# Performance work log

Hardware: AMD Instinct MI355X
Metric: run time of the kernel (lower is better)

The kernel has to match this reference:

```python
import jax, jax.numpy as jnp
import numpy as np

T, B, E, H = 1024, 8, 1024, 16
HD = E // H                       # 64
SCALE = float(HD * 1) ** -0.5     # scaling_factor = 1


def setup_inputs() -> dict:
    key = jax.random.key(0)
    ks = jax.random.split(key, 7)
    s = 0.02
    return {
        "query": jax.random.normal(ks[0], (T, B, E), jnp.float32),
        "key_padding_mask": jax.random.bernoulli(ks[1], 0.1, (B, T)),
        "attn_bias": jax.random.normal(ks[2], (1, H, T, T), jnp.float32) * 0.1,
        "wq": jax.random.normal(ks[3], (1, E, E), jnp.float32) * s,
        "wk": jax.random.normal(ks[4], (1, E, E), jnp.float32) * s,
        "wv": jax.random.normal(ks[5], (1, E, E), jnp.float32) * s,
        "wo": jax.random.normal(ks[6], (1, E, E), jnp.float32) * s,
    }


def _group_linear(x, w):
    # x: (T, B, nb*din), w: (nb, din, dout) -> (T, B, nb*dout). nb=1 here.
    t, b, _ = x.shape
    nb, din, dout = w.shape
    y = jnp.einsum('xnd,nde->xne', x.reshape(t * b, nb, din), w)
    return y.reshape(t, b, nb * dout)


def reference(query, key_padding_mask, attn_bias, wq, wk, wv, wo):
    q = _group_linear(query, wq) * SCALE
    k = _group_linear(query, wk)
    v = _group_linear(query, wv)

    # (T, B, E) -> (B*H, T, HD), matching torch view+transpose
    def split_heads(x):
        return x.reshape(T, B * H, HD).transpose(1, 0, 2)

    q, k, v = split_heads(q), split_heads(k), split_heads(v)

    scores = jnp.einsum('bth,bsh->bts', q, k).reshape(B, H, T, T)
    scores = scores + attn_bias
    scores = jnp.where(key_padding_mask[:, None, None, :], -jnp.inf, scores)
    probs = jax.nn.softmax(scores.astype(jnp.float32), axis=-1).astype(query.dtype)

    vh = v.reshape(B, H, T, HD)  # (B*H,T,HD) -> (B,H,S,HD)
    attn = jnp.einsum('bhts,bhsd->tbhd', probs, vh).reshape(T, B, H * HD)
    return _group_linear(attn, wo)
```

## Files before the change

kernel.cpp:

```cpp
#include <hip/hip_runtime.h>


typedef __bf16 bf16x8 __attribute__((ext_vector_type(8)));
typedef float f32x4 __attribute__((ext_vector_type(4)));

#define LOG2E 1.4426950408889634f
#define QSCALE 0.18033688011112042f

static __device__ __forceinline__ unsigned short f2bf_rn(float f) {
  union { float f; unsigned u; } x;
  x.f = f;
  unsigned r = (x.u + 0x7fffu + ((x.u >> 16) & 1u)) >> 16;
  return (unsigned short)r;
}
static __device__ __forceinline__ unsigned short f2bf(float f) {
  union { float f; unsigned u; } x;
  x.f = f;
  return (unsigned short)((x.u + 0x8000u) >> 16);
}

static __device__ __forceinline__ void async_cp16(const void* g, void* l) {
  __builtin_amdgcn_global_load_lds((__attribute__((address_space(1))) void*)g,
                                   (__attribute__((address_space(3))) void*)l,
                                   16, 0, 0);
}

__global__ void k_cvt(const float* __restrict__ src, unsigned short* __restrict__ dst) {
  const int idx = blockIdx.x * 256 + threadIdx.x;
  const float4 f = ((const float4*)src)[idx];
  unsigned lo = (unsigned)f2bf_rn(f.x) | ((unsigned)f2bf_rn(f.y) << 16);
  unsigned hi = (unsigned)f2bf_rn(f.z) | ((unsigned)f2bf_rn(f.w) << 16);
  uint2 v; v.x = lo; v.y = hi;
  *(uint2*)(dst + (size_t)idx * 4) = v;
}

__global__ void k_transw(const float* __restrict__ src, unsigned short* __restrict__ dst) {
  __shared__ float tile[32][33];
  const int bx = blockIdx.x << 5;
  const int by = blockIdx.y << 5;
  const int tx = threadIdx.x, ty = threadIdx.y;
#pragma unroll
  for (int i = 0; i < 32; i += 8)
    tile[ty + i][tx] = src[(size_t)(by + ty + i) * 1024 + bx + tx];
  __syncthreads();
#pragma unroll
  for (int i = 0; i < 32; i += 8)
    dst[(size_t)(bx + ty + i) * 1024 + by + tx] = f2bf_rn(tile[tx][ty + i]);
}

__global__ __launch_bounds__(256, 2) void k_biasT(const float* __restrict__ bias,
                                                  unsigned short* __restrict__ B2) {
  __shared__ unsigned short tile[128 * 132];
  const int tid = threadIdx.x;
  const int ss = blockIdx.x, tt = blockIdx.y, h = blockIdx.z;
  const float* src = bias + ((long)h * 1024 + tt * 128) * 1024 + ss * 128;
#pragma unroll
  for (int c = 0; c < 16; ++c) {
    int flat = c * 256 + tid;
    int row = flat >> 5, col = (flat & 31) << 2;
    float4 v = *(const float4*)(src + (long)row * 1024 + col);
    unsigned short* t4 = &tile[row * 132 + col];
    t4[0] = f2bf_rn(v.x * LOG2E); t4[1] = f2bf_rn(v.y * LOG2E);
    t4[2] = f2bf_rn(v.z * LOG2E); t4[3] = f2bf_rn(v.w * LOG2E);
  }
  __syncthreads();
  const int wid = tid >> 6, lane = tid & 63, lanelo = lane & 15, quad = lane >> 4;
  unsigned short outv[64];
#pragma unroll
  for (int mi = 0; mi < 2; ++mi)
#pragma unroll
    for (int nj = 0; nj < 8; ++nj)
#pragma unroll
      for (int r = 0; r < 4; ++r)
        outv[mi * 32 + nj * 4 + r] =
            tile[(wid * 32 + mi * 16 + quad * 4 + r) * 132 + nj * 16 + lanelo];
  unsigned short* dst = B2 + ((((long)(h * 8 + tt) * 8 + ss) * 256 + tid) << 6);
#pragma unroll
  for (int i = 0; i < 8; ++i) ((uint4*)dst)[i] = ((const uint4*)outv)[i];
}

static __device__ __forceinline__ void gemm_tile_128x128(
    const unsigned short* __restrict__ A, const unsigned short* __restrict__ Bt,
    int K, long m0, long n0,
    unsigned short* As, unsigned short* Bs, f32x4 acc[4][4]) {
  const int tid = threadIdx.x;
  const int wid = tid >> 6;
  const int lane = tid & 63;
  const int lanelo = lane & 15;
  const int quad = lane >> 4;
  const int wm = (wid >> 1) << 6;
  const int wn = (wid & 1) << 6;
  const int srow = tid >> 2;
  const int scol = (tid & 3) << 3;

  for (int k0 = 0; k0 < K; k0 += 32) {
    __syncthreads();
    {
      const unsigned short* ga0 = A + (m0 + srow) * K + k0 + scol;
      const unsigned short* ga1 = A + (m0 + srow + 64) * K + k0 + scol;
      const unsigned short* gb0 = Bt + (n0 + srow) * K + k0 + scol;
      const unsigned short* gb1 = Bt + (n0 + srow + 64) * K + k0 + scol;
      char* la = (char*)As + wid * 1024;
      char* lb = (char*)Bs + wid * 1024;
      async_cp16(ga0, la);
      async_cp16(ga1, la + 4096);
      async_cp16(gb0, lb);
      async_cp16(gb1, lb + 4096);
    }
    __syncthreads();
    bf16x8 a[4], b[4];
#pragma unroll
    for (int i = 0; i < 4; ++i) {
      a[i] = *(const bf16x8*)(As + (wm + i * 16 + lanelo) * 32 + quad * 8);
      b[i] = *(const bf16x8*)(Bs + (wn + i * 16 + lanelo) * 32 + quad * 8);
    }
#pragma unroll
    for (int i = 0; i < 4; ++i)
#pragma unroll
      for (int j = 0; j < 4; ++j)
        acc[i][j] = __builtin_amdgcn_mfma_f32_16x16x32_bf16(a[i], b[j], acc[i][j], 0, 0, 0);
  }
}

__global__ __launch_bounds__(256, 2) void k_gemm_qkv(
    const unsigned short* __restrict__ A, const unsigned short* __restrict__ Bt,
    unsigned short* __restrict__ Qh, unsigned short* __restrict__ Kh,
    unsigned short* __restrict__ Vt) {
  __shared__ unsigned short smem[9216];
  unsigned short* As = smem;
  unsigned short* Bs = smem + 4096;
  f32x4 acc[4][4];
  const f32x4 z4 = {0.f, 0.f, 0.f, 0.f};
#pragma unroll
  for (int i = 0; i < 4; ++i)
#pragma unroll
    for (int j = 0; j < 4; ++j) acc[i][j] = z4;

  const long m0 = (long)blockIdx.y * 128;
  const long n0 = (long)blockIdx.x * 128;
  gemm_tile_128x128(A, Bt, 1024, m0, n0, As, Bs, acc);

  const int tid = threadIdx.x;
  const int wid = tid >> 6;
  const int lane = tid & 63;
  const int lanelo = lane & 15;
  const int quad = lane >> 4;
  const int wm = (wid >> 1) << 6;
  const int wn = (wid & 1) << 6;
  const int which = (int)(blockIdx.x >> 3);

  if (which == 2) {
    unsigned short* Vt_s = smem;
    const long t0g = m0 >> 3;
#pragma unroll
    for (int half = 0; half < 2; ++half) {
      __syncthreads();
      if ((wid & 1) == half) {
#pragma unroll
        for (int mi = 0; mi < 4; ++mi)
#pragma unroll
          for (int nj = 0; nj < 4; ++nj)
#pragma unroll
            for (int r = 0; r < 4; ++r)
              Vt_s[(wm + mi * 16 + quad * 4 + r) * 72 + nj * 16 + lanelo] =
                  f2bf(acc[mi][nj][r]);
      }
      __syncthreads();
      const int h = (((int)(n0 & 1023)) >> 6) + half;
#pragma unroll
      for (int pp = 0; pp < 2; ++pp) {
        int p = tid + pp * 256;
        int b = p >> 6, d = p & 63;
        long off = ((long)(b * 16 + h)) << 16;
        __attribute__((aligned(16))) unsigned short vals[16];
#pragma unroll
        for (int t = 0; t < 16; ++t) vals[t] = Vt_s[(t * 8 + b) * 72 + d];
        uint4* dst = (uint4*)(Vt + off + (long)d * 1024 + t0g);
        dst[0] = ((const uint4*)vals)[0];
        dst[1] = ((const uint4*)vals)[1];
      }
    }
  } else {
#pragma unroll
    for (int mi = 0; mi < 4; ++mi)
#pragma unroll
      for (int nj = 0; nj < 4; ++nj)
#pragma unroll
        for (int r = 0; r < 4; ++r) {
          int m = (int)m0 + wm + mi * 16 + quad * 4 + r;
          int n = (int)n0 + wn + nj * 16 + lanelo;
          float v = acc[mi][nj][r];
          int t = m >> 3, b = m & 7;
          int e = n & 1023, h = e >> 6, d = e & 63;
          long off = ((long)(b * 16 + h)) << 16;
          if (which == 0)
            Qh[off + t * 64 + d] = f2bf(v * QSCALE);
          else
            Kh[off + t * 64 + d] = f2bf(v);
        }
  }
}

__global__ __launch_bounds__(256, 2) void k_attn(
    const unsigned short* __restrict__ Qh, const unsigned short* __restrict__ Kh,
    const unsigned short* __restrict__ Vt, const unsigned short* __restrict__ B2,
    const int* __restrict__ mask, unsigned short* __restrict__ A2) {
  __shared__ unsigned short Ks[128 * 72];
  __shared__ unsigned short Vs[64 * 136];
  __shared__ unsigned short Ps[128 * 136];
  __shared__ float Mf[1024];

  const int tid = threadIdx.x;
  const int wid = tid >> 6;
  const int lane = tid & 63;
  const int lanelo = lane & 15;
  const int quad = lane >> 4;
  const int bh = blockIdx.x;
  const int b = bh >> 4, h = bh & 15;
  const int tt = blockIdx.y;
  const int t0 = tt * 128;
  const long head = (long)bh << 16;

  {
    int4 mv = ((const int4*)(mask + (long)b * 1024))[tid];
    float4 f;
    f.x = mv.x ? -1e30f : 0.f;
    f.y = mv.y ? -1e30f : 0.f;
    f.z = mv.z ? -1e30f : 0.f;
    f.w = mv.w ? -1e30f : 0.f;
    *(float4*)&Mf[tid * 4] = f;
  }

  bf16x8 aq[2][2];
#pragma unroll
  for (int mi = 0; mi < 2; ++mi)
#pragma unroll
    for (int ks = 0; ks < 2; ++ks)
      aq[mi][ks] = *(const bf16x8*)(Qh + head +
                                    (long)(t0 + wid * 32 + mi * 16 + lanelo) * 64 +
                                    ks * 32 + quad * 8);

  const f32x4 z4 = {0.f, 0.f, 0.f, 0.f};
  f32x4 Oacc[2][4];
#pragma unroll
  for (int mi = 0; mi < 2; ++mi)
#pragma unroll
    for (int dj = 0; dj < 4; ++dj) Oacc[mi][dj] = z4;
  float mrow[2][4], lrow[2][4];
#pragma unroll
  for (int mi = 0; mi < 2; ++mi)
#pragma unroll
    for (int r = 0; r < 4; ++r) { mrow[mi][r] = -1e30f; lrow[mi][r] = 0.f; }

  const long biasbase = (((long)(h * 8 + tt) * 8) * 256 + tid) << 6;

  for (int s0 = 0; s0 < 1024; s0 += 128) {
    bf16x8 bfr[8];
    {
      const bf16x8* bp8 = (const bf16x8*)(B2 + biasbase + ((long)(s0 >> 7) * 256 << 6));
#pragma unroll
      for (int i = 0; i < 8; ++i) bfr[i] = bp8[i];
    }
    __syncthreads();
#pragma unroll
    for (int c = 0; c < 4; ++c) {
      int flat = c * 2048 + tid * 8;
      int row = flat >> 6, col = flat & 63;
      uint4 v = *(const uint4*)(Kh + head + (long)(s0 + row) * 64 + col);
      *(uint4*)&Ks[row * 72 + col] = v;
    }
#pragma unroll
    for (int c = 0; c < 4; ++c) {
      int flat = c * 2048 + tid * 8;
      int row = flat >> 7, col = flat & 127;
      uint4 v = *(const uint4*)(Vt + head + (long)row * 1024 + s0 + col);
      *(uint4*)&Vs[row * 136 + col] = v;
    }
    __syncthreads();

    f32x4 S[2][8];
#pragma unroll
    for (int mi = 0; mi < 2; ++mi)
#pragma unroll
      for (int nj = 0; nj < 8; ++nj) S[mi][nj] = z4;
#pragma unroll
    for (int ks = 0; ks < 2; ++ks) {
      bf16x8 bk[8];
#pragma unroll
      for (int nj = 0; nj < 8; ++nj)
        bk[nj] = *(const bf16x8*)(Ks + (nj * 16 + lanelo) * 72 + ks * 32 + quad * 8);
#pragma unroll
      for (int mi = 0; mi < 2; ++mi)
#pragma unroll
        for (int nj = 0; nj < 8; ++nj)
          S[mi][nj] = __builtin_amdgcn_mfma_f32_16x16x32_bf16(aq[mi][ks], bk[nj], S[mi][nj], 0, 0, 0);
    }

    float madd[8];
#pragma unroll
    for (int nj = 0; nj < 8; ++nj) madd[nj] = Mf[s0 + nj * 16 + lanelo];
#pragma unroll
    for (int mi = 0; mi < 2; ++mi)
#pragma unroll
      for (int nj = 0; nj < 8; ++nj)
#pragma unroll
        for (int r = 0; r < 4; ++r)
          S[mi][nj][r] += (float)bfr[mi * 4 + (nj >> 1)][(nj & 1) * 4 + r] + madd[nj];

#pragma unroll
    for (int mi = 0; mi < 2; ++mi)
#pragma unroll
      for (int r = 0; r < 4; ++r) {
        float mx = -1e30f;
#pragma unroll
        for (int nj = 0; nj < 8; ++nj) mx = fmaxf(mx, S[mi][nj][r]);
        mx = fmaxf(mx, __shfl_xor(mx, 1, 16));
        mx = fmaxf(mx, __shfl_xor(mx, 2, 16));
        mx = fmaxf(mx, __shfl_xor(mx, 4, 16));
        mx = fmaxf(mx, __shfl_xor(mx, 8, 16));
        float mold = mrow[mi][r];
        float mnew = fmaxf(mold, mx);
        float al = exp2f(mold - mnew);
        mrow[mi][r] = mnew;
        float rs = 0.f;
#pragma unroll
        for (int nj = 0; nj < 8; ++nj) {
          float p = exp2f(S[mi][nj][r] - mnew);
          S[mi][nj][r] = p;
          rs += p;
        }
        rs += __shfl_xor(rs, 1, 16);
        rs += __shfl_xor(rs, 2, 16);
        rs += __shfl_xor(rs, 4, 16);
        rs += __shfl_xor(rs, 8, 16);
        lrow[mi][r] = lrow[mi][r] * al + rs;
#pragma unroll
        for (int dj = 0; dj < 4; ++dj) Oacc[mi][dj][r] *= al;
      }

#pragma unroll
    for (int mi = 0; mi < 2; ++mi)
#pragma unroll
      for (int nj = 0; nj < 8; ++nj)
#pragma unroll
        for (int r = 0; r < 4; ++r)
          Ps[(wid * 32 + mi * 16 + quad * 4 + r) * 136 + nj * 16 + lanelo] =
              f2bf(S[mi][nj][r]);

#pragma unroll
    for (int ks = 0; ks < 4; ++ks) {
      bf16x8 ap[2];
#pragma unroll
      for (int mi = 0; mi < 2; ++mi)
        ap[mi] = *(const bf16x8*)(Ps + (wid * 32 + mi * 16 + lanelo) * 136 + ks * 32 + quad * 8);
      bf16x8 bv[4];
#pragma unroll
      for (int dj = 0; dj < 4; ++dj)
        bv[dj] = *(const bf16x8*)(Vs + (dj * 16 + lanelo) * 136 + ks * 32 + quad * 8);
#pragma unroll
      for (int mi = 0; mi < 2; ++mi)
#pragma unroll
        for (int dj = 0; dj < 4; ++dj)
          Oacc[mi][dj] = __builtin_amdgcn_mfma_f32_16x16x32_bf16(ap[mi], bv[dj], Oacc[mi][dj], 0, 0, 0);
    }
  }

#pragma unroll
  for (int mi = 0; mi < 2; ++mi)
#pragma unroll
    for (int r = 0; r < 4; ++r) {
      float rinv = __builtin_amdgcn_rcpf(lrow[mi][r]);
      int t = t0 + wid * 32 + mi * 16 + quad * 4 + r;
#pragma unroll
      for (int dj = 0; dj < 4; ++dj) {
        int d = dj * 16 + lanelo;
        A2[(long)(t * 8 + b) * 1024 + h * 64 + d] = f2bf(Oacc[mi][dj][r] * rinv);
      }
    }
}

__global__ __launch_bounds__(256, 2) void k_gemm_out(
    const unsigned short* __restrict__ A, const unsigned short* __restrict__ Bt,
    float* __restrict__ out) {
  __shared__ unsigned short As[128 * 32];
  __shared__ unsigned short Bs[128 * 32];
  f32x4 acc[4][4];
  const f32x4 z4 = {0.f, 0.f, 0.f, 0.f};
#pragma unroll
  for (int i = 0; i < 4; ++i)
#pragma unroll
    for (int j = 0; j < 4; ++j) acc[i][j] = z4;

  const long m0 = (long)blockIdx.y * 128;
  const long n0 = (long)blockIdx.x * 128;
  gemm_tile_128x128(A, Bt, 1024, m0, n0, As, Bs, acc);

  const int tid = threadIdx.x;
  const int wid = tid >> 6;
  const int lane = tid & 63;
  const int lanelo = lane & 15;
  const int quad = lane >> 4;
  const int wm = (wid >> 1) << 6;
  const int wn = (wid & 1) << 6;
#pragma unroll
  for (int mi = 0; mi < 4; ++mi)
#pragma unroll
    for (int nj = 0; nj < 4; ++nj)
#pragma unroll
      for (int r = 0; r < 4; ++r) {
        long m = m0 + wm + mi * 16 + quad * 4 + r;
        long n = n0 + wn + nj * 16 + lanelo;
        out[m * 1024 + n] = acc[mi][nj][r];
      }
}

extern "C" void kernel_launch(void* const* d_in, const int* in_sizes, int n_in,
                              void* d_out, int out_size, void* d_ws, size_t ws_size,
                              hipStream_t stream) {
  const float* query = (const float*)d_in[0];
  const int* mask = (const int*)d_in[1];
  const float* bias = (const float*)d_in[2];
  const float* wq = (const float*)d_in[3];
  const float* wk = (const float*)d_in[4];
  const float* wv = (const float*)d_in[5];
  const float* wo = (const float*)d_in[6];
  float* out = (float*)d_out;

  char* ws = (char*)d_ws;
  const size_t MB = 1024 * 1024;
  unsigned short* Abuf  = (unsigned short*)(ws);
  unsigned short* WqkvT = (unsigned short*)(ws + 16 * MB);
  unsigned short* WoT   = (unsigned short*)(ws + 22 * MB);
  unsigned short* Qh    = (unsigned short*)(ws + 24 * MB);
  unsigned short* Kh    = (unsigned short*)(ws + 40 * MB);
  unsigned short* Vt    = (unsigned short*)(ws + 56 * MB);
  unsigned short* A2    = (unsigned short*)(ws + 72 * MB);
  unsigned short* B2    = (unsigned short*)(ws + 88 * MB);

  k_cvt<<<dim3(8192), dim3(256), 0, stream>>>(query, Abuf);
  dim3 tb(32, 8);
  k_transw<<<dim3(32, 32), tb, 0, stream>>>(wq, WqkvT);
  k_transw<<<dim3(32, 32), tb, 0, stream>>>(wk, WqkvT + 1024 * 1024);
  k_transw<<<dim3(32, 32), tb, 0, stream>>>(wv, WqkvT + 2 * 1024 * 1024);
  k_transw<<<dim3(32, 32), tb, 0, stream>>>(wo, WoT);
  k_biasT<<<dim3(8, 8, 16), dim3(256), 0, stream>>>(bias, B2);
  k_gemm_qkv<<<dim3(24, 64), dim3(256), 0, stream>>>(Abuf, WqkvT, Qh, Kh, Vt);
  k_attn<<<dim3(128, 8), dim3(256), 0, stream>>>(Qh, Kh, Vt, B2, mask, A2);
  k_gemm_out<<<dim3(8, 64), dim3(256), 0, stream>>>(A2, WoT, out);
}
```

Before: 407.4 us.

## Shrink attention LDS footprint and precompute key mask to raise occupancy

The P tile in shared memory is halved by staging softmax probabilities in two 64-column halves, each consumed by the PV matmul before the next is written. The per-block mask-to-float conversion moves into a separate small kernel and is read from global memory each KV tile. The attention kernel's launch bound rises to 3 blocks per CU. This aims for more resident blocks, at the cost of a tighter register budget, an extra tiny launch, and extra global mask loads.

Measured after the change: 515.9 us. +26.6%, slower.

```diff
diff --git a/kernel.cpp b/kernel.cpp
--- a/kernel.cpp
+++ b/kernel.cpp
@@ -32,6 +32,11 @@
   unsigned hi = (unsigned)f2bf_rn(f.z) | ((unsigned)f2bf_rn(f.w) << 16);
   uint2 v; v.x = lo; v.y = hi;
   *(uint2*)(dst + (size_t)idx * 4) = v;
+}
+
+__global__ void k_mask(const int* __restrict__ mask, float* __restrict__ Mfg) {
+  const int i = blockIdx.x * 256 + threadIdx.x;
+  Mfg[i] = mask[i] ? -1e30f : 0.f;
 }
 
 __global__ void k_transw(const float* __restrict__ src, unsigned short* __restrict__ dst) {
@@ -201,14 +206,13 @@
   }
 }
 
-__global__ __launch_bounds__(256, 2) void k_attn(
+__global__ __launch_bounds__(256, 3) void k_attn(
     const unsigned short* __restrict__ Qh, const unsigned short* __restrict__ Kh,
     const unsigned short* __restrict__ Vt, const unsigned short* __restrict__ B2,
-    const int* __restrict__ mask, unsigned short* __restrict__ A2) {
+    const float* __restrict__ Mfg, unsigned short* __restrict__ A2) {
   __shared__ unsigned short Ks[128 * 72];
   __shared__ unsigned short Vs[64 * 136];
-  __shared__ unsigned short Ps[128 * 136];
-  __shared__ float Mf[1024];
+  __shared__ unsigned short Ps[128 * 72];
 
   const int tid = threadIdx.x;
   const int wid = tid >> 6;
@@ -221,16 +225,6 @@
   const int t0 = tt * 128;
   const long head = (long)bh << 16;
 
-  {
-    int4 mv = ((const int4*)(mask + (long)b * 1024))[tid];
-    float4 f;
-    f.x = mv.x ? -1e30f : 0.f;
-    f.y = mv.y ? -1e30f : 0.f;
-    f.z = mv.z ? -1e30f : 0.f;
-    f.w = mv.w ? -1e30f : 0.f;
-    *(float4*)&Mf[tid * 4] = f;
-  }
-
   bf16x8 aq[2][2];
 #pragma unroll
   for (int mi = 0; mi < 2; ++mi)
@@ -261,6 +255,11 @@
 #pragma unroll
       for (int i = 0; i < 8; ++i) bfr[i] = bp8[i];
     }
+    float madd[8];
+#pragma unroll
+    for (int nj = 0; nj < 8; ++nj)
+      madd[nj] = Mfg[(long)b * 1024 + s0 + nj * 16 + lanelo];
+
     __syncthreads();
 #pragma unroll
     for (int c = 0; c < 4; ++c) {
@@ -296,9 +295,6 @@
           S[mi][nj] = __builtin_amdgcn_mfma_f32_16x16x32_bf16(aq[mi][ks], bk[nj], S[mi][nj], 0, 0, 0);
     }
 
-    float madd[8];
-#pragma unroll
-    for (int nj = 0; nj < 8; ++nj) madd[nj] = Mf[s0 + nj * 16 + lanelo];
 #pragma unroll
     for (int mi = 0; mi < 2; ++mi)
 #pragma unroll
@@ -339,29 +335,31 @@
       }
 
 #pragma unroll
-    for (int mi = 0; mi < 2; ++mi)
-#pragma unroll
-      for (int nj = 0; nj < 8; ++nj)
-#pragma unroll
-        for (int r = 0; r < 4; ++r)
-          Ps[(wid * 32 + mi * 16 + quad * 4 + r) * 136 + nj * 16 + lanelo] =
-              f2bf(S[mi][nj][r]);
-
-#pragma unroll
-    for (int ks = 0; ks < 4; ++ks) {
-      bf16x8 ap[2];
+    for (int half = 0; half < 2; ++half) {
 #pragma unroll
       for (int mi = 0; mi < 2; ++mi)
-        ap[mi] = *(const bf16x8*)(Ps + (wid * 32 + mi * 16 + lanelo) * 136 + ks * 32 + quad * 8);
-      bf16x8 bv[4];
-#pragma unroll
-      for (int dj = 0; dj < 4; ++dj)
-        bv[dj] = *(const bf16x8*)(Vs + (dj * 16 + lanelo) * 136 + ks * 32 + quad * 8);
-#pragma unroll
-      for (int mi = 0; mi < 2; ++mi)
+#pragma unroll
+        for (int njl = 0; njl < 4; ++njl)
+#pragma unroll
+          for (int r = 0; r < 4; ++r)
+            Ps[(wid * 32 + mi * 16 + quad * 4 + r) * 72 + njl * 16 + lanelo] =
+                f2bf(S[mi][half * 4 + njl][r]);
+#pragma unroll
+      for (int ks2 = 0; ks2 < 2; ++ks2) {
+        const int ks = half * 2 + ks2;
+        bf16x8 ap[2], bv[4];
+#pragma unroll
+        for (int mi = 0; mi < 2; ++mi)
+          ap[mi] = *(const bf16x8*)(Ps + (wid * 32 + mi * 16 + lanelo) * 72 + ks2 * 32 + quad * 8);
 #pragma unroll
         for (int dj = 0; dj < 4; ++dj)
-          Oacc[mi][dj] = __builtin_amdgcn_mfma_f32_16x16x32_bf16(ap[mi], bv[dj], Oacc[mi][dj], 0, 0, 0);
+          bv[dj] = *(const bf16x8*)(Vs + (dj * 16 + lanelo) * 136 + ks * 32 + quad * 8);
+#pragma unroll
+        for (int mi = 0; mi < 2; ++mi)
+#pragma unroll
+          for (int dj = 0; dj < 4; ++dj)
+            Oacc[mi][dj] = __builtin_amdgcn_mfma_f32_16x16x32_bf16(ap[mi], bv[dj], Oacc[mi][dj], 0, 0, 0);
+      }
     }
   }
 
@@ -436,8 +434,10 @@
   unsigned short* Vt    = (unsigned short*)(ws + 56 * MB);
   unsigned short* A2    = (unsigned short*)(ws + 72 * MB);
   unsigned short* B2    = (unsigned short*)(ws + 88 * MB);
+  float*          Mfg   = (float*)(ws + 120 * MB);
 
   k_cvt<<<dim3(8192), dim3(256), 0, stream>>>(query, Abuf);
+  k_mask<<<dim3(32), dim3(256), 0, stream>>>(mask, Mfg);
   dim3 tb(32, 8);
   k_transw<<<dim3(32, 32), tb, 0, stream>>>(wq, WqkvT);
   k_transw<<<dim3(32, 32), tb, 0, stream>>>(wk, WqkvT + 1024 * 1024);
@@ -445,6 +445,6 @@
   k_transw<<<dim3(32, 32), tb, 0, stream>>>(wo, WoT);
   k_biasT<<<dim3(8, 8, 16), dim3(256), 0, stream>>>(bias, B2);
   k_gemm_qkv<<<dim3(24, 64), dim3(256), 0, stream>>>(Abuf, WqkvT, Qh, Kh, Vt);
-  k_attn<<<dim3(128, 8), dim3(256), 0, stream>>>(Qh, Kh, Vt, B2, mask, A2);
+  k_attn<<<dim3(128, 8), dim3(256), 0, stream>>>(Qh, Kh, Vt, B2, Mfg, A2);
   k_gemm_out<<<dim3(8, 64), dim3(256), 0, stream>>>(A2, WoT, out);
 }
```
